# Kernel optimization log

Measured on AMD Instinct MI355X. Metric: run time of the kernel, lower is better.

Reference implementation:

```python
import jax, jax.numpy as jnp
import numpy as np

N, E = 40000, 640000
DIN, HID, H = 512, 128, 4
C = HID  # per-head channels; H*C == 512 == DIN
BN_EPS = 1e-5


def setup_inputs() -> dict:
    key = jax.random.key(0)
    ks = jax.random.split(key, 32)
    sc = 0.05
    d = {}
    d["x"] = jax.random.normal(ks[0], (N, DIN), jnp.float32)
    d["edge_index"] = jax.random.randint(ks[1], (2, E), 0, N)
    i = 2
    for l in (1, 2, 3):
        d[f"W{l}"] = jax.random.normal(ks[i], (DIN, H * C), jnp.float32) * sc; i += 1
        d[f"as{l}"] = jax.random.normal(ks[i], (H, C), jnp.float32) * sc; i += 1
        d[f"ad{l}"] = jax.random.normal(ks[i], (H, C), jnp.float32) * sc; i += 1
        d[f"b{l}"] = jnp.zeros((H * C,), jnp.float32)
        d[f"g{l}"] = jnp.ones((H * C,), jnp.float32)
        d[f"be{l}"] = jnp.zeros((H * C,), jnp.float32)
    d["Wg1"] = jax.random.normal(ks[i], (H * C, HID), jnp.float32) * sc; i += 1
    d["bg1"] = jnp.zeros((HID,), jnp.float32)
    d["Wg2"] = jax.random.normal(ks[i], (HID, 1), jnp.float32) * sc; i += 1
    d["bg2"] = jnp.zeros((1,), jnp.float32)
    d["Wf1"] = jax.random.normal(ks[i], (H * C, HID), jnp.float32) * sc; i += 1
    d["bf1"] = jnp.zeros((HID,), jnp.float32)
    d["Wf2"] = jax.random.normal(ks[i], (HID, HID), jnp.float32) * sc; i += 1
    d["bf2"] = jnp.zeros((HID,), jnp.float32)
    d["Wp"] = jax.random.normal(ks[i], (HID + H * C, HID), jnp.float32) * sc; i += 1
    d["bp"] = jnp.zeros((HID,), jnp.float32)
    return d


def _gat(x, src, dst, W, a_s, a_d, b):
    # PyG GATConv (concat=True, negative_slope=0.2, self-loops already in src/dst)
    n = x.shape[0]
    h = (x @ W).reshape(n, H, C)                      # [N,H,C]
    es = jnp.einsum('nhc,hc->nh', h, a_s)             # alpha_src per node
    ed = jnp.einsum('nhc,hc->nh', h, a_d)             # alpha_dst per node
    e = jax.nn.leaky_relu(es[src] + ed[dst], 0.2)     # [Etot,H]
    m = jax.ops.segment_max(e, dst, num_segments=n)   # softmax over incoming edges
    ex = jnp.exp(e - m[dst])
    s = jax.ops.segment_sum(ex, dst, num_segments=n)
    w = ex / (s[dst] + 1e-16)                         # [Etot,H]
    out = jax.ops.segment_sum(w[:, :, None] * h[src], dst, num_segments=n)
    return out.reshape(n, H * C) + b


def _bn(x, g, b):
    mu = x.mean(0)
    var = x.var(0)
    return (x - mu) * jax.lax.rsqrt(var + BN_EPS) * g + b


def reference(x, edge_index,
              W1, as1, ad1, b1, g1, be1,
              W2, as2, ad2, b2, g2, be2,
              W3, as3, ad3, b3, g3, be3,
              Wg1, bg1, Wg2, bg2, Wf1, bf1, Wf2, bf2, Wp, bp):
    n = x.shape[0]
    loops = jnp.arange(n)
    src = jnp.concatenate([edge_index[0], loops])
    dst = jnp.concatenate([edge_index[1], loops])

    h = jax.nn.leaky_relu(_bn(_gat(x, src, dst, W1, as1, ad1, b1), g1, be1), 0.2)
    h_res = h
    h = jax.nn.leaky_relu(_bn(_gat(h, src, dst, W2, as2, ad2, b2), g2, be2), 0.2) + h_res
    h_res = h
    h = jax.nn.leaky_relu(_bn(_gat(h, src, dst, W3, as3, ad3, b3), g3, be3), 0.2) + h_res

    attn_scores = (jnp.tanh(h @ Wg1 + bg1) @ Wg2 + bg2)[:, 0]   # [N]
    attn_w = jax.nn.softmax(attn_scores)                        # softmax over all nodes
    feat = jax.nn.relu(h @ Wf1 + bf1) @ Wf2 + bf2               # [N,HID]
    gated = (attn_w[:, None] * feat).sum(0)                     # [HID]
    global_pooled = h.mean(0, keepdims=True)                    # batch=None -> one graph
    combined = jnp.concatenate([gated[None, :], global_pooled], axis=-1)  # [1,640]
    out = (combined @ Wp + bp)[0]                               # [HID]
    return out, attn_scores
```

## Files before the change

### kernel.cpp

```cpp
#include <hip/hip_runtime.h>
#include <math.h>

#define N_NODES 40000
#define M_PAD   40064
#define N_EDGES 640000
#define ETOT    (N_EDGES + N_NODES)
#define DINC    512
#define NHEAD   4
#define CHD     128
#define BN_EPS  1e-5f

typedef __attribute__((ext_vector_type(8))) short bf16x8;
typedef __attribute__((ext_vector_type(4))) float f32x4;

static __device__ __forceinline__ float lrelu(float x) { return x > 0.f ? x : 0.2f * x; }

static __device__ __forceinline__ unsigned short f2b(float f) {
    union { float f; unsigned int u; } v; v.f = f;
    unsigned int r = (v.u + 0x7fff + ((v.u >> 16) & 1)) >> 16;
    return (unsigned short)r;
}
static __device__ __forceinline__ float b2f(unsigned short b) {
    union { unsigned int u; float f; } v; v.u = ((unsigned int)b) << 16;
    return v.f;
}
static __device__ __forceinline__ float lo16(unsigned int u) {
    union { unsigned int u; float f; } v; v.u = u << 16; return v.f;
}
static __device__ __forceinline__ float hi16(unsigned int u) {
    union { unsigned int u; float f; } v; v.u = u & 0xffff0000u; return v.f;
}

static __device__ __forceinline__ void fma8(float* acc, uint4 hv, float wgt) {
    acc[0] += wgt * lo16(hv.x); acc[1] += wgt * hi16(hv.x);
    acc[2] += wgt * lo16(hv.y); acc[3] += wgt * hi16(hv.y);
    acc[4] += wgt * lo16(hv.z); acc[5] += wgt * hi16(hv.z);
    acc[6] += wgt * lo16(hv.w); acc[7] += wgt * hi16(hv.w);
}

#define GLDS16(g, l) __builtin_amdgcn_global_load_lds( \
    (__attribute__((address_space(1))) void*)(g),      \
    (__attribute__((address_space(3))) void*)(l), 16, 0, 0)

#define CVTX_BLK 10000
#define PAD_QUADS 4096
__global__ __launch_bounds__(256) void k_prep(const float4* __restrict__ xin,
                                              uint4* __restrict__ xb,
                                              uint4* __restrict__ curb,
                                              uint4* __restrict__ cnt4) {
    int bid = blockIdx.x;
    int tid = threadIdx.x;
    if (bid < CVTX_BLK) {
        size_t i = (size_t)bid * 256 + tid;
        float4 a = xin[i * 2], b = xin[i * 2 + 1];
        uint4 o;
        o.x = (unsigned)f2b(a.x) | ((unsigned)f2b(a.y) << 16);
        o.y = (unsigned)f2b(a.z) | ((unsigned)f2b(a.w) << 16);
        o.z = (unsigned)f2b(b.x) | ((unsigned)f2b(b.y) << 16);
        o.w = (unsigned)f2b(b.z) | ((unsigned)f2b(b.w) << 16);
        xb[i] = o;
    } else if (bid < CVTX_BLK + 16) {
        int i = (bid - CVTX_BLK) * 256 + tid;
        xb[(size_t)N_NODES * DINC / 8 + i] = make_uint4(0, 0, 0, 0);
    } else if (bid < CVTX_BLK + 32) {
        int i = (bid - CVTX_BLK - 16) * 256 + tid;
        curb[(size_t)N_NODES * DINC / 8 + i] = make_uint4(0, 0, 0, 0);
    } else {
        int i = (bid - CVTX_BLK - 32) * 256 + tid;
        if (i < N_NODES / 4) cnt4[i] = make_uint4(0, 0, 0, 0);
    }
}

__global__ __launch_bounds__(256) void k_cvtw_all(const float* __restrict__ W1, unsigned short* __restrict__ T1,
                                                  const float* __restrict__ W2, unsigned short* __restrict__ T2,
                                                  const float* __restrict__ W3, unsigned short* __restrict__ T3,
                                                  const float* __restrict__ Wg1, const float* __restrict__ Wf1,
                                                  unsigned short* __restrict__ Wct) {
    int idx = blockIdx.x * 256 + threadIdx.x;
    const float* W; unsigned short* T; int Nn;
    if (idx < 262144)            { W = W1; T = T1; Nn = 512; }
    else if (idx < 524288)       { W = W2; T = T2; Nn = 512; idx -= 262144; }
    else if (idx < 786432)       { W = W3; T = T3; Nn = 512; idx -= 524288; }
    else if (idx < 851968)       { W = Wg1; T = Wct; Nn = 128; idx -= 786432; }
    else                         { W = Wf1; T = Wct + 65536; Nn = 128; idx -= 851968; }
    int k = idx / Nn, n = idx % Nn;
    T[(size_t)n * 512 + k] = f2b(W[idx]);
}

__global__ void k_degree(const int* __restrict__ ei, int* __restrict__ cnt) {
    int e = blockIdx.x * 256 + threadIdx.x;
    if (e < ETOT) {
        int dst = (e < N_EDGES) ? ei[N_EDGES + e] : (e - N_EDGES);
        atomicAdd(&cnt[dst], 1);
    }
}

__global__ __launch_bounds__(64) void k_scan1(const int* __restrict__ deg, int* __restrict__ bsum) {
    int lane = threadIdx.x;
    int v = deg[blockIdx.x * 64 + lane];
#pragma unroll
    for (int off = 32; off; off >>= 1) v += __shfl_xor(v, off);
    if (lane == 0) bsum[blockIdx.x] = v;
}

__global__ __launch_bounds__(64) void k_scan23(const int* __restrict__ deg, const int* __restrict__ bsum,
                                               int* __restrict__ rowptr, int* __restrict__ cnt) {
    int b = blockIdx.x, lane = threadIdx.x;
    int pre = 0;
    for (int i = lane; i < b; i += 64) pre += bsum[i];
#pragma unroll
    for (int off = 32; off; off >>= 1) pre += __shfl_xor(pre, off);
    int i = b * 64 + lane;
    int v = deg[i];
    int inc = v;
#pragma unroll
    for (int off = 1; off < 64; off <<= 1) {
        int t = __shfl_up(inc, off);
        if (lane >= off) inc += t;
    }
    rowptr[i] = pre + inc - v;
    cnt[i] = 0;
    if (b == 624 && lane == 63) rowptr[N_NODES] = ETOT;
}

__global__ void k_fill(const int* __restrict__ ei, const int* __restrict__ rowptr,
                       int* __restrict__ cnt, int* __restrict__ csr_src) {
    int e = blockIdx.x * 256 + threadIdx.x;
    if (e < ETOT) {
        int src, dst;
        if (e < N_EDGES) { src = ei[e]; dst = ei[N_EDGES + e]; }
        else             { src = e - N_EDGES; dst = src; }
        int pos = rowptr[dst] + atomicAdd(&cnt[dst], 1);
        csr_src[pos] = src;
    }
}

template<int CBF16, int EPI>
__global__ __launch_bounds__(256) void k_gemm_mfma(const unsigned short* __restrict__ A,
                                                   const unsigned short* __restrict__ Bt,
                                                   void* __restrict__ Cout,
                                                   int Nn, int K, int nbn,
                                                   const float* __restrict__ p1,
                                                   const float* __restrict__ p2,
                                                   float* __restrict__ p3,
                                                   float* __restrict__ p4,
                                                   const float* __restrict__ p5,
                                                   const float* __restrict__ p6) {
    __shared__ alignas(16) unsigned short As[128 * 64];
    __shared__ alignas(16) unsigned short Bs[128 * 64];
    const int tid  = threadIdx.x;
    const int wv   = tid >> 6;
    const int lane = tid & 63;
    const int bm = (blockIdx.x / nbn) * 128;
    const int bn = (blockIdx.x % nbn) * 128;
    const int wm = (wv >> 1) * 64;
    const int wn = (wv & 1) * 64;

    const int srow = lane >> 3;
    const int scol = (((lane & 7) ^ srow) * 8);
    const size_t a_base = (size_t)(bm + wv * 32 + srow) * K + scol;
    const size_t b_base = (size_t)(bn + wv * 32 + srow) * K + scol;

    f32x4 acc[4][4] = {};

    for (int k0 = 0; k0 < K; k0 += 64) {
#pragma unroll
        for (int q = 0; q < 4; ++q)
            GLDS16(A + a_base + (size_t)q * 8 * K + k0, &As[(wv * 32 + q * 8) * 64]);
#pragma unroll
        for (int q = 0; q < 4; ++q)
            GLDS16(Bt + b_base + (size_t)q * 8 * K + k0, &Bs[(wv * 32 + q * 8) * 64]);
        __syncthreads();

        const int r0 = lane & 15;
#pragma unroll
        for (int ks = 0; ks < 2; ++ks) {
            const int c = ks * 4 + (lane >> 4);
            bf16x8 af[4], bfr[4];
#pragma unroll
            for (int i = 0; i < 4; ++i) {
                int row = wm + i * 16 + r0;
                af[i] = *(const bf16x8*)&As[row * 64 + ((c ^ (row & 7)) * 8)];
            }
#pragma unroll
            for (int j = 0; j < 4; ++j) {
                int row = wn + j * 16 + r0;
                bfr[j] = *(const bf16x8*)&Bs[row * 64 + ((c ^ (row & 7)) * 8)];
            }
#pragma unroll
            for (int i = 0; i < 4; ++i)
#pragma unroll
                for (int j = 0; j < 4; ++j)
                    acc[i][j] = __builtin_amdgcn_mfma_f32_16x16x32_bf16(af[i], bfr[j], acc[i][j], 0, 0, 0);
        }
        __syncthreads();
    }

    const int crow0 = bm + wm + (lane >> 4) * 4;
    const int ccol  = bn + wn + (lane & 15);

    if (EPI != 2) {
#pragma unroll
        for (int i = 0; i < 4; ++i)
#pragma unroll
            for (int j = 0; j < 4; ++j)
#pragma unroll
                for (int r = 0; r < 4; ++r) {
                    size_t off = (size_t)(crow0 + i * 16 + r) * Nn + ccol + j * 16;
                    if (CBF16) ((unsigned short*)Cout)[off] = f2b(acc[i][j][r]);
                    else       ((float*)Cout)[off] = acc[i][j][r];
                }
    }

    if (EPI == 1) {
        const int head = bn >> 7;
        float asv[4], adv[4];
#pragma unroll
        for (int j = 0; j < 4; ++j) {
            int cc = head * CHD + wn + j * 16 + (lane & 15);
            asv[j] = p1[cc];
            adv[j] = p2[cc];
        }
        float* sE = (float*)As;
        sE[tid] = 0.f;
        __syncthreads();
#pragma unroll
        for (int i = 0; i < 4; ++i)
#pragma unroll
            for (int r = 0; r < 4; ++r) {
                float e = acc[i][0][r] * asv[0] + acc[i][1][r] * asv[1]
                        + acc[i][2][r] * asv[2] + acc[i][3][r] * asv[3];
                float d = acc[i][0][r] * adv[0] + acc[i][1][r] * adv[1]
                        + acc[i][2][r] * adv[2] + acc[i][3][r] * adv[3];
#pragma unroll
                for (int off = 8; off; off >>= 1) {
                    e += __shfl_xor(e, off);
                    d += __shfl_xor(d, off);
                }
                if ((lane & 15) == 0) {
                    int rloc = wm + i * 16 + (lane >> 4) * 4 + r;
                    atomicAdd(&sE[rloc], e);
                    atomicAdd(&sE[128 + rloc], d);
                }
            }
        __syncthreads();
        if (tid < 128) {
            p3[(size_t)(bm + tid) * NHEAD + head] = sE[tid];
            p4[(size_t)(bm + tid) * NHEAD + head] = sE[128 + tid];
        }
    }

    if (EPI == 2) {
        if (bn == 0) {
            float wgv[4], bgv[4];
#pragma unroll
            for (int j = 0; j < 4; ++j) {
                int cc = wn + j * 16 + (lane & 15);
                bgv[j] = p1[cc];
                wgv[j] = p2[cc];
            }
            float* sE = (float*)As;
            sE[tid] = 0.f;
            __syncthreads();
#pragma unroll
            for (int i = 0; i < 4; ++i)
#pragma unroll
                for (int r = 0; r < 4; ++r) {
                    float e = tanhf(acc[i][0][r] + bgv[0]) * wgv[0]
                            + tanhf(acc[i][1][r] + bgv[1]) * wgv[1]
                            + tanhf(acc[i][2][r] + bgv[2]) * wgv[2]
                            + tanhf(acc[i][3][r] + bgv[3]) * wgv[3];
#pragma unroll
                    for (int off = 8; off; off >>= 1) e += __shfl_xor(e, off);
                    if ((lane & 15) == 0)
                        atomicAdd(&sE[wm + i * 16 + (lane >> 4) * 4 + r], e);
                }
            __syncthreads();
            if (tid < 128) p3[bm + tid] = sE[tid] + p5[0];
        } else {
#pragma unroll
            for (int j = 0; j < 4; ++j) {
                int colF = wn + j * 16 + (lane & 15);
                float bv = p6[colF];
#pragma unroll
                for (int i = 0; i < 4; ++i)
#pragma unroll
                    for (int r = 0; r < 4; ++r)
                        p4[(size_t)(crow0 + i * 16 + r) * 128 + colF] =
                            fmaxf(acc[i][j][r] + bv, 0.f);
            }
        }
    }
}

__global__ __launch_bounds__(256) void k_mxi(const float4* __restrict__ es4,
                                             const float4* __restrict__ ed4,
                                             const int* __restrict__ rowptr,
                                             const int* __restrict__ csr_src,
                                             float4* __restrict__ mx4,
                                             float4* __restrict__ inv4,
                                             float* __restrict__ stats) {
    if (blockIdx.x == 0)
        for (int q = threadIdx.x; q < DINC * 2; q += 256) stats[q] = 0.f;
    int n = blockIdx.x * 4 + (threadIdx.x >> 6);
    int lane = threadIdx.x & 63;
    int start = rowptr[n], end = rowptr[n + 1];
    float4 edn = ed4[n];
    float4 mx = make_float4(-1e30f, -1e30f, -1e30f, -1e30f);
    for (int j0 = start; j0 < end; j0 += 64) {
        int j = j0 + lane;
        if (j < end) {
            int s = csr_src[j];
            float4 e = es4[s];
            mx.x = fmaxf(mx.x, lrelu(e.x + edn.x));
            mx.y = fmaxf(mx.y, lrelu(e.y + edn.y));
            mx.z = fmaxf(mx.z, lrelu(e.z + edn.z));
            mx.w = fmaxf(mx.w, lrelu(e.w + edn.w));
        }
    }
#pragma unroll
    for (int off = 32; off; off >>= 1) {
        mx.x = fmaxf(mx.x, __shfl_xor(mx.x, off));
        mx.y = fmaxf(mx.y, __shfl_xor(mx.y, off));
        mx.z = fmaxf(mx.z, __shfl_xor(mx.z, off));
        mx.w = fmaxf(mx.w, __shfl_xor(mx.w, off));
    }
    float4 sum = make_float4(0.f, 0.f, 0.f, 0.f);
    for (int j0 = start; j0 < end; j0 += 64) {
        int j = j0 + lane;
        if (j < end) {
            int s = csr_src[j];
            float4 e = es4[s];
            sum.x += __expf(lrelu(e.x + edn.x) - mx.x);
            sum.y += __expf(lrelu(e.y + edn.y) - mx.y);
            sum.z += __expf(lrelu(e.z + edn.z) - mx.z);
            sum.w += __expf(lrelu(e.w + edn.w) - mx.w);
        }
    }
#pragma unroll
    for (int off = 32; off; off >>= 1) {
        sum.x += __shfl_xor(sum.x, off);
        sum.y += __shfl_xor(sum.y, off);
        sum.z += __shfl_xor(sum.z, off);
        sum.w += __shfl_xor(sum.w, off);
    }
    if (lane == 0) {
        mx4[n] = mx;
        float4 iv;
        iv.x = 1.f / (sum.x + 1e-16f);
        iv.y = 1.f / (sum.y + 1e-16f);
        iv.z = 1.f / (sum.z + 1e-16f);
        iv.w = 1.f / (sum.w + 1e-16f);
        inv4[n] = iv;
    }
}

__global__ __launch_bounds__(256) void k_agg(const unsigned short* __restrict__ hb,
                                             const float4* __restrict__ es4,
                                             const int* __restrict__ rowptr,
                                             const int* __restrict__ csr_src,
                                             const float* __restrict__ mxp,
                                             const float* __restrict__ invp,
                                             const float* __restrict__ edp,
                                             unsigned short* __restrict__ aggb) {
    __shared__ float part[4][512];
    const int n = blockIdx.x;
    const int tid = threadIdx.x;
    const int grp = tid >> 6;
    const int lane = tid & 63;
    const int head = lane >> 4;
    const int start = rowptr[n], end = rowptr[n + 1];
    const float mxh = mxp[n * NHEAD + head];
    const float ivh = invp[n * NHEAD + head];
    const float edh = edp[n * NHEAD + head];

    float acc[8] = {};
    int j = start + grp;
    int s_n = 0; float4 e_n = make_float4(0.f, 0.f, 0.f, 0.f);
    if (j < end) { s_n = csr_src[j]; e_n = es4[s_n]; }
    while (j < end) {
        int s = s_n; float4 e4 = e_n;
        int j2 = j + 4;
        if (j2 < end) { s_n = csr_src[j2]; e_n = es4[s_n]; }
        float esh = (head == 0) ? e4.x : (head == 1) ? e4.y : (head == 2) ? e4.z : e4.w;
        float wgt = __expf(lrelu(esh + edh) - mxh) * ivh;
        uint4 hv = *(const uint4*)&hb[(size_t)s * DINC + lane * 8];
        fma8(acc, hv, wgt);
        j = j2;
    }
    *(float4*)&part[grp][lane * 8]     = make_float4(acc[0], acc[1], acc[2], acc[3]);
    *(float4*)&part[grp][lane * 8 + 4] = make_float4(acc[4], acc[5], acc[6], acc[7]);
    __syncthreads();
    const int c = tid * 2;
    float v0 = part[0][c] + part[1][c] + part[2][c] + part[3][c];
    float v1 = part[0][c + 1] + part[1][c + 1] + part[2][c + 1] + part[3][c + 1];
    unsigned int o = (unsigned)f2b(v0) | ((unsigned)f2b(v1) << 16);
    *(unsigned int*)&aggb[(size_t)n * DINC + c] = o;
}

__global__ __launch_bounds__(256) void k_bn_stats(const unsigned short* __restrict__ aggb,
                                                  float* __restrict__ stats) {
    int tid = threadIdx.x;
    int row0 = blockIdx.x * 64;
    int c0 = tid * 2;
    float s0 = 0, q0 = 0, s1 = 0, q1 = 0;
    for (int r = row0; r < row0 + 64; ++r) {
        unsigned int hv = *(const unsigned int*)&aggb[(size_t)r * DINC + c0];
        float v0 = lo16(hv), v1 = hi16(hv);
        s0 += v0; q0 += v0 * v0;
        s1 += v1; q1 += v1 * v1;
    }
    atomicAdd(&stats[c0], s0);
    atomicAdd(&stats[c0 + 1], s1);
    atomicAdd(&stats[DINC + c0], q0);
    atomicAdd(&stats[DINC + c0 + 1], q1);
}

__global__ __launch_bounds__(512) void k_bn_fin(const float* __restrict__ stats,
                                                const float* __restrict__ g,
                                                const float* __restrict__ be,
                                                float* __restrict__ ab) {
    int c = threadIdx.x;
    float mu = stats[c] * (1.f / N_NODES);
    float var = stats[DINC + c] * (1.f / N_NODES) - mu * mu;
    float rstd = rsqrtf(var + BN_EPS);
    float A = g[c] * rstd;
    ab[c] = A;
    ab[DINC + c] = be[c] - mu * A;
}

__global__ __launch_bounds__(256) void k_bn_act(const unsigned short* __restrict__ aggb,
                                                const float* __restrict__ ab,
                                                unsigned short* __restrict__ curb,
                                                int res) {
    size_t idx = (size_t)blockIdx.x * 256 + threadIdx.x;
    int c8 = ((int)(idx & 63)) * 8;
    uint4 v = *(const uint4*)&aggb[idx * 8];
    float xv[8] = { lo16(v.x), hi16(v.x), lo16(v.y), hi16(v.y),
                    lo16(v.z), hi16(v.z), lo16(v.w), hi16(v.w) };
#pragma unroll
    for (int q = 0; q < 8; ++q)
        xv[q] = lrelu(xv[q] * ab[c8 + q] + ab[DINC + c8 + q]);
    if (res) {
        uint4 r = *(const uint4*)&curb[idx * 8];
        xv[0] += lo16(r.x); xv[1] += hi16(r.x);
        xv[2] += lo16(r.y); xv[3] += hi16(r.y);
        xv[4] += lo16(r.z); xv[5] += hi16(r.z);
        xv[6] += lo16(r.w); xv[7] += hi16(r.w);
    }
    uint4 o;
    o.x = (unsigned)f2b(xv[0]) | ((unsigned)f2b(xv[1]) << 16);
    o.y = (unsigned)f2b(xv[2]) | ((unsigned)f2b(xv[3]) << 16);
    o.z = (unsigned)f2b(xv[4]) | ((unsigned)f2b(xv[5]) << 16);
    o.w = (unsigned)f2b(xv[6]) | ((unsigned)f2b(xv[7]) << 16);
    *(uint4*)&curb[idx * 8] = o;
}

__global__ __launch_bounds__(1024) void k_softmax(const float* __restrict__ scores, float* __restrict__ sm,
                                                  float* __restrict__ vbuf, float* __restrict__ pooled) {
    __shared__ float red[16];
    int tid = threadIdx.x, lane = tid & 63, wv = tid >> 6;
    if (tid < 128) vbuf[tid] = 0.f;
    if (tid < DINC) pooled[tid] = 0.f;
    float m = -1e30f;
    for (int i = tid; i < N_NODES; i += 1024) m = fmaxf(m, scores[i]);
#pragma unroll
    for (int off = 32; off; off >>= 1) m = fmaxf(m, __shfl_xor(m, off));
    if (lane == 0) red[wv] = m;
    __syncthreads();
    float mall = red[0];
    for (int i = 1; i < 16; ++i) mall = fmaxf(mall, red[i]);
    __syncthreads();
    float s = 0.f;
    for (int i = tid; i < N_NODES; i += 1024) s += expf(scores[i] - mall);
#pragma unroll
    for (int off = 32; off; off >>= 1) s += __shfl_xor(s, off);
    if (lane == 0) red[wv] = s;
    __syncthreads();
    if (tid == 0) {
        float tot = 0.f;
        for (int i = 0; i < 16; ++i) tot += red[i];
        sm[0] = mall; sm[1] = tot;
    }
}

__global__ __launch_bounds__(640) void k_vpool(const float* __restrict__ Fb,
                                               const unsigned short* __restrict__ hb,
                                               const float* __restrict__ scores,
                                               const float* __restrict__ sm,
                                               float* __restrict__ v,
                                               float* __restrict__ pooled) {
    int tid = threadIdx.x;
    int row0 = blockIdx.x * 64;
    float mall = sm[0];
    float invS = 1.f / sm[1];
    if (tid < 128) {
        float acc = 0.f;
        for (int r = row0; r < row0 + 64; ++r) {
            float w = expf(scores[r] - mall) * invS;
            acc += w * Fb[(size_t)r * 128 + tid];
        }
        atomicAdd(&v[tid], acc);
    } else {
        int c = tid - 128;
        float acc = 0.f;
        for (int r = row0; r < row0 + 64; ++r) acc += b2f(hb[(size_t)r * DINC + c]);
        atomicAdd(&pooled[c], acc * (1.f / N_NODES));
    }
}

__global__ __launch_bounds__(128) void k_final(const float* __restrict__ v,
                                               const float* __restrict__ pooled,
                                               const float* __restrict__ Wf2,
                                               const float* __restrict__ bf2,
                                               const float* __restrict__ Wp,
                                               const float* __restrict__ bp,
                                               float* __restrict__ out) {
    __shared__ float sg[128];
    int o = threadIdx.x;
    float g = bf2[o];
    for (int k = 0; k < 128; ++k) g += v[k] * Wf2[k * 128 + o];
    sg[o] = g;
    __syncthreads();
    float acc = bp[o];
    for (int c = 0; c < 128; ++c) acc += sg[c] * Wp[c * 128 + o];
    for (int j = 0; j < 512; ++j) acc += pooled[j] * Wp[(128 + j) * 128 + o];
    out[o] = acc;
}

extern "C" void kernel_launch(void* const* d_in, const int* in_sizes, int n_in,
                              void* d_out, int out_size, void* d_ws, size_t ws_size,
                              hipStream_t stream) {
    const float* x  = (const float*)d_in[0];
    const int*   ei = (const int*)d_in[1];
    const float* Wg1 = (const float*)d_in[20];
    const float* bg1 = (const float*)d_in[21];
    const float* Wg2 = (const float*)d_in[22];
    const float* bg2 = (const float*)d_in[23];
    const float* Wf1 = (const float*)d_in[24];
    const float* bf1 = (const float*)d_in[25];
    const float* Wf2 = (const float*)d_in[26];
    const float* bf2 = (const float*)d_in[27];
    const float* Wp  = (const float*)d_in[28];
    const float* bp  = (const float*)d_in[29];
    float* out = (float*)d_out;

    char* base = (char*)d_ws;
    size_t off = 0;
    auto take = [&](size_t nbytes) -> char* {
        char* p = base + off;
        off += (nbytes + 255) & ~(size_t)255;
        return p;
    };
    unsigned short* hb   = (unsigned short*)take((size_t)M_PAD * DINC * 2);
    unsigned short* curb = (unsigned short*)take((size_t)M_PAD * DINC * 2);
    unsigned short* xb   = (unsigned short*)take((size_t)M_PAD * DINC * 2);
    unsigned short* aggb = (unsigned short*)take((size_t)M_PAD * DINC * 2);
    float* Fb    = (float*)take((size_t)M_PAD * 128 * 4);
    float* es    = (float*)take((size_t)M_PAD * NHEAD * 4);
    float* ed    = (float*)take((size_t)M_PAD * NHEAD * 4);
    float* mxp   = (float*)take((size_t)N_NODES * NHEAD * 4);
    float* invp  = (float*)take((size_t)N_NODES * NHEAD * 4);
    int*   rowptr= (int*)take((size_t)(N_NODES + 1) * 4);
    int*   cnt   = (int*)take((size_t)N_NODES * 4);
    int*   csr   = (int*)take((size_t)ETOT * 4);
    int*   bsum  = (int*)take(625 * 4);
    float* stats = (float*)take(DINC * 2 * 4);
    float* ab    = (float*)take(DINC * 2 * 4);
    float* sm    = (float*)take(2 * 4);
    float* vbuf  = (float*)take(128 * 4);
    float* pooled= (float*)take(DINC * 4);
    unsigned short* Wt1  = (unsigned short*)take((size_t)DINC * DINC * 2);
    unsigned short* Wt2  = (unsigned short*)take((size_t)DINC * DINC * 2);
    unsigned short* Wt3  = (unsigned short*)take((size_t)DINC * DINC * 2);
    unsigned short* Wct  = (unsigned short*)take((size_t)256 * DINC * 2);

    k_prep<<<CVTX_BLK + 32 + 40, 256, 0, stream>>>((const float4*)x, (uint4*)xb,
                                                   (uint4*)curb, (uint4*)cnt);
    k_cvtw_all<<<3584, 256, 0, stream>>>((const float*)d_in[2], Wt1,
                                         (const float*)d_in[8], Wt2,
                                         (const float*)d_in[14], Wt3,
                                         Wg1, Wf1, Wct);
    k_degree<<<(ETOT + 255) / 256, 256, 0, stream>>>(ei, cnt);
    k_scan1<<<625, 64, 0, stream>>>(cnt, bsum);
    k_scan23<<<625, 64, 0, stream>>>(cnt, bsum, rowptr, cnt);
    k_fill<<<(ETOT + 255) / 256, 256, 0, stream>>>(ei, rowptr, cnt, csr);

    const unsigned short* Wts[3] = {Wt1, Wt2, Wt3};
    const unsigned short* in = xb;
    for (int l = 0; l < 3; ++l) {
        const float* as_ = (const float*)d_in[2 + l * 6 + 1];
        const float* ad_ = (const float*)d_in[2 + l * 6 + 2];
        const float* g   = (const float*)d_in[2 + l * 6 + 4];
        const float* be  = (const float*)d_in[2 + l * 6 + 5];

        k_gemm_mfma<1, 1><<<(M_PAD / 128) * (DINC / 128), 256, 0, stream>>>(
            in, Wts[l], hb, DINC, DINC, DINC / 128, as_, ad_, es, ed, nullptr, nullptr);
        k_mxi<<<N_NODES / 4, 256, 0, stream>>>((const float4*)es, (const float4*)ed, rowptr, csr,
                                               (float4*)mxp, (float4*)invp, stats);
        k_agg<<<N_NODES, 256, 0, stream>>>(hb, (const float4*)es, rowptr, csr,
                                           mxp, invp, ed, aggb);
        k_bn_stats<<<N_NODES / 64, 256, 0, stream>>>(aggb, stats);
        k_bn_fin<<<1, 512, 0, stream>>>(stats, g, be, ab);
        k_bn_act<<<(N_NODES * (DINC / 8)) / 256, 256, 0, stream>>>(aggb, ab, curb, l > 0 ? 1 : 0);
        in = curb;
    }

    float* scores = out + 128;
    k_gemm_mfma<0, 2><<<(M_PAD / 128) * 2, 256, 0, stream>>>(
        curb, Wct, nullptr, 256, DINC, 2, bg1, Wg2, scores, Fb, bg2, bf1);

    k_softmax<<<1, 1024, 0, stream>>>(scores, sm, vbuf, pooled);
    k_vpool<<<N_NODES / 64, 640, 0, stream>>>(Fb, curb, scores, sm, vbuf, pooled);
    k_final<<<1, 128, 0, stream>>>(vbuf, pooled, Wf2, bf2, Wp, bp, out);
}
```

Baseline: 916.6 us.

## Precompute per-edge softmax weights and fold BN finalize into activation kernel

The softmax pass now writes unnormalized per-edge exp weights to a buffer. The aggregation kernel reads those weights directly instead of gathering es and recomputing exp, and applies the 1/sum normalization once per output element. The separate BN finalize kernel is removed and each thread of the activation kernel recomputes mean, variance and scale from the stats, saving one launch per layer. The cost is an extra ETOT*16-byte weight buffer written and read each layer, plus redundant per-element BN arithmetic.

```diff
diff --git a/kernel.cpp b/kernel.cpp
--- a/kernel.cpp
+++ b/kernel.cpp
@@ -43,7 +43,6 @@
     (__attribute__((address_space(3))) void*)(l), 16, 0, 0)
 
 #define CVTX_BLK 10000
-#define PAD_QUADS 4096
 __global__ __launch_bounds__(256) void k_prep(const float4* __restrict__ xin,
                                               uint4* __restrict__ xb,
                                               uint4* __restrict__ curb,
@@ -293,11 +292,11 @@
     }
 }
 
-__global__ __launch_bounds__(256) void k_mxi(const float4* __restrict__ es4,
+__global__ __launch_bounds__(256) void k_wts(const float4* __restrict__ es4,
                                              const float4* __restrict__ ed4,
                                              const int* __restrict__ rowptr,
                                              const int* __restrict__ csr_src,
-                                             float4* __restrict__ mx4,
+                                             float4* __restrict__ wbuf4,
                                              float4* __restrict__ inv4,
                                              float* __restrict__ stats) {
     if (blockIdx.x == 0)
@@ -331,10 +330,13 @@
         if (j < end) {
             int s = csr_src[j];
             float4 e = es4[s];
-            sum.x += __expf(lrelu(e.x + edn.x) - mx.x);
-            sum.y += __expf(lrelu(e.y + edn.y) - mx.y);
-            sum.z += __expf(lrelu(e.z + edn.z) - mx.z);
-            sum.w += __expf(lrelu(e.w + edn.w) - mx.w);
+            float4 ex;
+            ex.x = __expf(lrelu(e.x + edn.x) - mx.x);
+            ex.y = __expf(lrelu(e.y + edn.y) - mx.y);
+            ex.z = __expf(lrelu(e.z + edn.z) - mx.z);
+            ex.w = __expf(lrelu(e.w + edn.w) - mx.w);
+            wbuf4[j] = ex;
+            sum.x += ex.x; sum.y += ex.y; sum.z += ex.z; sum.w += ex.w;
         }
     }
 #pragma unroll
@@ -345,7 +347,6 @@
         sum.w += __shfl_xor(sum.w, off);
     }
     if (lane == 0) {
-        mx4[n] = mx;
         float4 iv;
         iv.x = 1.f / (sum.x + 1e-16f);
         iv.y = 1.f / (sum.y + 1e-16f);
@@ -356,12 +357,10 @@
 }
 
 __global__ __launch_bounds__(256) void k_agg(const unsigned short* __restrict__ hb,
-                                             const float4* __restrict__ es4,
                                              const int* __restrict__ rowptr,
                                              const int* __restrict__ csr_src,
-                                             const float* __restrict__ mxp,
+                                             const float* __restrict__ wbuf,
                                              const float* __restrict__ invp,
-                                             const float* __restrict__ edp,
                                              unsigned short* __restrict__ aggb) {
     __shared__ float part[4][512];
     const int n = blockIdx.x;
@@ -370,20 +369,15 @@
     const int lane = tid & 63;
     const int head = lane >> 4;
     const int start = rowptr[n], end = rowptr[n + 1];
-    const float mxh = mxp[n * NHEAD + head];
-    const float ivh = invp[n * NHEAD + head];
-    const float edh = edp[n * NHEAD + head];
 
     float acc[8] = {};
     int j = start + grp;
-    int s_n = 0; float4 e_n = make_float4(0.f, 0.f, 0.f, 0.f);
-    if (j < end) { s_n = csr_src[j]; e_n = es4[s_n]; }
+    int s_n = 0; float w_n = 0.f;
+    if (j < end) { s_n = csr_src[j]; w_n = wbuf[j * 4 + head]; }
     while (j < end) {
-        int s = s_n; float4 e4 = e_n;
+        int s = s_n; float wgt = w_n;
         int j2 = j + 4;
-        if (j2 < end) { s_n = csr_src[j2]; e_n = es4[s_n]; }
-        float esh = (head == 0) ? e4.x : (head == 1) ? e4.y : (head == 2) ? e4.z : e4.w;
-        float wgt = __expf(lrelu(esh + edh) - mxh) * ivh;
+        if (j2 < end) { s_n = csr_src[j2]; w_n = wbuf[j2 * 4 + head]; }
         uint4 hv = *(const uint4*)&hb[(size_t)s * DINC + lane * 8];
         fma8(acc, hv, wgt);
         j = j2;
@@ -394,6 +388,8 @@
     const int c = tid * 2;
     float v0 = part[0][c] + part[1][c] + part[2][c] + part[3][c];
     float v1 = part[0][c + 1] + part[1][c + 1] + part[2][c + 1] + part[3][c + 1];
+    float iv = invp[(n << 2) + (c >> 7)];
+    v0 *= iv; v1 *= iv;
     unsigned int o = (unsigned)f2b(v0) | ((unsigned)f2b(v1) << 16);
     *(unsigned int*)&aggb[(size_t)n * DINC + c] = o;
 }
@@ -416,21 +412,10 @@
     atomicAdd(&stats[DINC + c0 + 1], q1);
 }
 
-__global__ __launch_bounds__(512) void k_bn_fin(const float* __restrict__ stats,
+__global__ __launch_bounds__(256) void k_bn_act(const unsigned short* __restrict__ aggb,
+                                                const float* __restrict__ stats,
                                                 const float* __restrict__ g,
                                                 const float* __restrict__ be,
-                                                float* __restrict__ ab) {
-    int c = threadIdx.x;
-    float mu = stats[c] * (1.f / N_NODES);
-    float var = stats[DINC + c] * (1.f / N_NODES) - mu * mu;
-    float rstd = rsqrtf(var + BN_EPS);
-    float A = g[c] * rstd;
-    ab[c] = A;
-    ab[DINC + c] = be[c] - mu * A;
-}
-
-__global__ __launch_bounds__(256) void k_bn_act(const unsigned short* __restrict__ aggb,
-                                                const float* __restrict__ ab,
                                                 unsigned short* __restrict__ curb,
                                                 int res) {
     size_t idx = (size_t)blockIdx.x * 256 + threadIdx.x;
@@ -439,8 +424,14 @@
     float xv[8] = { lo16(v.x), hi16(v.x), lo16(v.y), hi16(v.y),
                     lo16(v.z), hi16(v.z), lo16(v.w), hi16(v.w) };
 #pragma unroll
-    for (int q = 0; q < 8; ++q)
-        xv[q] = lrelu(xv[q] * ab[c8 + q] + ab[DINC + c8 + q]);
+    for (int q = 0; q < 8; ++q) {
+        int c = c8 + q;
+        float mu = stats[c] * (1.f / N_NODES);
+        float var = stats[DINC + c] * (1.f / N_NODES) - mu * mu;
+        float A = g[c] * rsqrtf(var + BN_EPS);
+        float B = be[c] - mu * A;
+        xv[q] = lrelu(xv[q] * A + B);
+    }
     if (res) {
         uint4 r = *(const uint4*)&curb[idx * 8];
         xv[0] += lo16(r.x); xv[1] += hi16(r.x);
@@ -559,14 +550,13 @@
     float* Fb    = (float*)take((size_t)M_PAD * 128 * 4);
     float* es    = (float*)take((size_t)M_PAD * NHEAD * 4);
     float* ed    = (float*)take((size_t)M_PAD * NHEAD * 4);
-    float* mxp   = (float*)take((size_t)N_NODES * NHEAD * 4);
+    float* wbuf  = (float*)take((size_t)ETOT * NHEAD * 4);
     float* invp  = (float*)take((size_t)N_NODES * NHEAD * 4);
     int*   rowptr= (int*)take((size_t)(N_NODES + 1) * 4);
     int*   cnt   = (int*)take((size_t)N_NODES * 4);
     int*   csr   = (int*)take((size_t)ETOT * 4);
     int*   bsum  = (int*)take(625 * 4);
     float* stats = (float*)take(DINC * 2 * 4);
-    float* ab    = (float*)take(DINC * 2 * 4);
     float* sm    = (float*)take(2 * 4);
     float* vbuf  = (float*)take(128 * 4);
     float* pooled= (float*)take(DINC * 4);
@@ -596,13 +586,11 @@
 
         k_gemm_mfma<1, 1><<<(M_PAD / 128) * (DINC / 128), 256, 0, stream>>>(
             in, Wts[l], hb, DINC, DINC, DINC / 128, as_, ad_, es, ed, nullptr, nullptr);
-        k_mxi<<<N_NODES / 4, 256, 0, stream>>>((const float4*)es, (const float4*)ed, rowptr, csr,
-                                               (float4*)mxp, (float4*)invp, stats);
-        k_agg<<<N_NODES, 256, 0, stream>>>(hb, (const float4*)es, rowptr, csr,
-                                           mxp, invp, ed, aggb);
+        k_wts<<<N_NODES / 4, 256, 0, stream>>>((const float4*)es, (const float4*)ed, rowptr, csr,
+                                               (float4*)wbuf, (float4*)invp, stats);
+        k_agg<<<N_NODES, 256, 0, stream>>>(hb, rowptr, csr, wbuf, invp, aggb);
         k_bn_stats<<<N_NODES / 64, 256, 0, stream>>>(aggb, stats);
-        k_bn_fin<<<1, 512, 0, stream>>>(stats, g, be, ab);
-        k_bn_act<<<(N_NODES * (DINC / 8)) / 256, 256, 0, stream>>>(aggb, ab, curb, l > 0 ? 1 : 0);
+        k_bn_act<<<(N_NODES * (DINC / 8)) / 256, 256, 0, stream>>>(aggb, stats, g, be, curb, l > 0 ? 1 : 0);
         in = curb;
     }
 
```

Measured after the change: 891.6 us. -2.7%, faster.
